# Optimization experiments

Measured on AMD Instinct MI355X. Metric: run time of the kernel, lower is better.

The kernel has to match this reference:

```python
import jax, jax.numpy as jnp
import numpy as np

N, IN_DIM, KEY_DIM, K, VAL_DIM = 100000, 512, 100, 8, 64


def setup_inputs() -> dict:
    key = jax.random.key(0)
    ks = jax.random.split(key, 7)
    s = 0.02
    return {
        "x": jax.random.normal(ks[0], (N, IN_DIM), dtype=jnp.float32),
        "Wk": jax.random.normal(ks[1], (KEY_DIM, IN_DIM), dtype=jnp.float32) * s,
        "bk": jax.random.normal(ks[2], (KEY_DIM,), dtype=jnp.float32) * s,
        "Wq": jax.random.normal(ks[3], (K, KEY_DIM), dtype=jnp.float32) * s,
        "bq": jax.random.normal(ks[4], (K,), dtype=jnp.float32) * s,
        "Wv": jax.random.normal(ks[5], (VAL_DIM, IN_DIM), dtype=jnp.float32) * s,
        "bv": jax.random.normal(ks[6], (VAL_DIM,), dtype=jnp.float32) * s,
    }


def reference(x, Wk, bk, Wq, bq, Wv, bv):
    # torch.nn.Linear: y = x @ W.T + b
    key = x @ Wk.T + bk                  # [N, key_dim]
    val = x @ Wv.T + bv                  # [N, val_dim]
    que = key @ Wq.T + bq                # [N, k]
    # att_norm == 'softmax': per-sample softmax over the k groups
    w = jax.nn.softmax(que, axis=-1)     # [N, k]
    # per-sample outer product w_i^T @ val_i -> [N, k, val_dim]
    x_group = w[:, :, None] * val[:, None, :]
    return x_group
```

## Files before the change

kernel.cpp:

```cpp
#include <hip/hip_runtime.h>

#define NROWS 100000
#define IN_DIM 512

typedef __attribute__((ext_vector_type(8))) short short8;
typedef __attribute__((ext_vector_type(4))) float f32x4;

__device__ inline unsigned short f2bf(float f) {
    union { float f; unsigned u; } v; v.f = f;
    unsigned u = v.u;
    return (unsigned short)((u + 0x7FFFu + ((u >> 16) & 1u)) >> 16);
}

__global__ void qg_prepack(const float* __restrict__ Wk, const float* __restrict__ bk,
                           const float* __restrict__ Wq, const float* __restrict__ bq,
                           const float* __restrict__ Wv,
                           unsigned short* __restrict__ Bp, float* __restrict__ qb) {
    int id = blockIdx.x * 256 + threadIdx.x;
    if (id < 8) {
        float s = bq[id];
        #pragma unroll 4
        for (int j = 0; j < 100; ++j) s += Wq[id * 100 + j] * bk[j];
        qb[id] = s;
    }
    if (id >= 5120) return;
    int lane = id & 63;
    int ks = (id >> 6) & 15;
    int t = id >> 10;
    int c = t * 16 + (lane & 15);
    int kk = ks * 32 + (lane >> 4) * 8;
    short8 pk;
    #pragma unroll
    for (int e = 0; e < 8; ++e) {
        int k2 = kk + e;
        float w;
        if (c < 64) {
            w = Wv[c * IN_DIM + k2];
        } else if (c < 72) {
            float s = 0.f;
            #pragma unroll 4
            for (int j = 0; j < 100; ++j) s += Wq[(c - 64) * 100 + j] * Wk[j * IN_DIM + k2];
            w = s;
        } else {
            w = 0.f;
        }
        pk[e] = (short)f2bf(w);
    }
    ((short8*)Bp)[id] = pk;
}

__global__ __launch_bounds__(128, 4) void qg_main(const float* __restrict__ x,
                                                  const float* __restrict__ bv,
                                                  const unsigned short* __restrict__ Bp,
                                                  const float* __restrict__ qb,
                                                  float* __restrict__ out) {
    __shared__ float vlds[2][16][68];
    __shared__ float wlds[2][16][8];
    const int tid = threadIdx.x;
    const int w = tid >> 6;
    const int lane = tid & 63;
    const int g = lane >> 4;
    const int cl = lane & 15;
    const int rowbase = blockIdx.x * 32 + w * 16;

    const float* ap = x + (size_t)(rowbase + cl) * IN_DIM + g * 8;
    const short8* bp8 = (const short8*)Bp + lane;

    f32x4 acc[5];
    #pragma unroll
    for (int t = 0; t < 5; ++t) acc[t] = (f32x4){0.f, 0.f, 0.f, 0.f};

    float4 A[3][2];
    short8 B[2][5];

    #pragma unroll
    for (int p = 0; p < 3; ++p) {
        A[p][0] = *(const float4*)(ap + p * 32);
        A[p][1] = *(const float4*)(ap + p * 32 + 4);
    }
    #pragma unroll
    for (int p = 0; p < 2; ++p)
        #pragma unroll
        for (int t = 0; t < 5; ++t)
            B[p][t] = bp8[(t * 16 + p) * 64];

    #pragma unroll
    for (int s = 0; s < 16; ++s) {
        const int ai = s % 3, bi = s % 2;
        float4 f0 = A[ai][0];
        float4 f1 = A[ai][1];
        short8 af;
        af[0] = (short)f2bf(f0.x); af[1] = (short)f2bf(f0.y);
        af[2] = (short)f2bf(f0.z); af[3] = (short)f2bf(f0.w);
        af[4] = (short)f2bf(f1.x); af[5] = (short)f2bf(f1.y);
        af[6] = (short)f2bf(f1.z); af[7] = (short)f2bf(f1.w);
        if (s + 3 < 16) {
            A[ai][0] = *(const float4*)(ap + (s + 3) * 32);
            A[ai][1] = *(const float4*)(ap + (s + 3) * 32 + 4);
        }
        #pragma unroll
        for (int t = 0; t < 5; ++t)
            acc[t] = __builtin_amdgcn_mfma_f32_16x16x32_bf16(af, B[bi][t], acc[t], 0, 0, 0);
        if (s + 2 < 16) {
            #pragma unroll
            for (int t = 0; t < 5; ++t)
                B[bi][t] = bp8[(t * 16 + s + 2) * 64];
        }
    }

    #pragma unroll
    for (int t = 0; t < 4; ++t) {
        float b = bv[t * 16 + cl];
        #pragma unroll
        for (int r = 0; r < 4; ++r)
            vlds[w][g * 4 + r][t * 16 + cl] = acc[t][r] + b;
    }
    if (cl < 8) {
        float b = qb[cl];
        #pragma unroll
        for (int r = 0; r < 4; ++r)
            wlds[w][g * 4 + r][cl] = acc[4][r] + b;
    }
    asm volatile("s_waitcnt lgkmcnt(0)" ::: "memory");

    if (lane < 16) {
        float q[8];
        float m = -1e30f;
        #pragma unroll
        for (int k = 0; k < 8; ++k) { q[k] = wlds[w][lane][k]; m = fmaxf(m, q[k]); }
        float ssum = 0.f;
        #pragma unroll
        for (int k = 0; k < 8; ++k) { q[k] = __expf(q[k] - m); ssum += q[k]; }
        float inv = 1.f / ssum;
        #pragma unroll
        for (int k = 0; k < 8; ++k) wlds[w][lane][k] = q[k] * inv;
    }
    asm volatile("s_waitcnt lgkmcnt(0)" ::: "memory");

    f32x4* outp = (f32x4*)out + (size_t)rowbase * 128;
    #pragma unroll
    for (int it = 0; it < 32; ++it) {
        int idx = it * 64 + lane;
        int row = idx >> 7;
        int j = idx & 127;
        float wgt = wlds[w][row][j >> 4];
        float4 vv = *(const float4*)&vlds[w][row][(j & 15) * 4];
        f32x4 o;
        o[0] = wgt * vv.x; o[1] = wgt * vv.y; o[2] = wgt * vv.z; o[3] = wgt * vv.w;
        __builtin_nontemporal_store(o, &outp[(size_t)row * 128 + j]);
    }
}

extern "C" void kernel_launch(void* const* d_in, const int* in_sizes, int n_in,
                              void* d_out, int out_size, void* d_ws, size_t ws_size,
                              hipStream_t stream) {
    const float* x  = (const float*)d_in[0];
    const float* Wk = (const float*)d_in[1];
    const float* bk = (const float*)d_in[2];
    const float* Wq = (const float*)d_in[3];
    const float* bq = (const float*)d_in[4];
    const float* Wv = (const float*)d_in[5];
    const float* bv = (const float*)d_in[6];
    float* out = (float*)d_out;

    unsigned short* Bp = (unsigned short*)d_ws;
    float* qb = (float*)((char*)d_ws + 81920);

    qg_prepack<<<20, 256, 0, stream>>>(Wk, bk, Wq, bq, Wv, Bp, qb);
    qg_main<<<3125, 128, 0, stream>>>(x, bv, Bp, qb, out);
}
```

Measured before the change: 107.1 us.

## Rewrite main GEMM loop in inline asm with 64-row warp tiles

Each wave now processes 64 rows (four 16-row M tiles) instead of 16, so every B fragment load is reused across four MFMA groups. The K loop is hand-written in inline assembly with pinned VGPRs, double-buffered global loads, explicit vmcnt waits and packed bf16 conversion instructions in place of the software rounding. The grid shrinks to 782 blocks and the rows past the end are clamped on load and masked on store. Hard-coded register clobbers and inline asm waits are fragile, and dropping to 2 blocks per CU lowers the occupancy available to hide memory latency in what is a bandwidth-bound kernel.

```diff
diff --git a/kernel.cpp b/kernel.cpp
--- a/kernel.cpp
+++ b/kernel.cpp
@@ -49,105 +49,237 @@
     ((short8*)Bp)[id] = pk;
 }
 
-__global__ __launch_bounds__(128, 4) void qg_main(const float* __restrict__ x,
+#define C32_63  "v32","v33","v34","v35","v36","v37","v38","v39","v40","v41","v42","v43","v44","v45","v46","v47","v48","v49","v50","v51","v52","v53","v54","v55","v56","v57","v58","v59","v60","v61","v62","v63"
+#define C64_95  "v64","v65","v66","v67","v68","v69","v70","v71","v72","v73","v74","v75","v76","v77","v78","v79","v80","v81","v82","v83","v84","v85","v86","v87","v88","v89","v90","v91","v92","v93","v94","v95"
+#define C96_135 "v96","v97","v98","v99","v100","v101","v102","v103","v104","v105","v106","v107","v108","v109","v110","v111","v112","v113","v114","v115","v116","v117","v118","v119","v120","v121","v122","v123","v124","v125","v126","v127","v128","v129","v130","v131","v132","v133","v134","v135"
+#define C136_175 "v136","v137","v138","v139","v140","v141","v142","v143","v144","v145","v146","v147","v148","v149","v150","v151","v152","v153","v154","v155","v156","v157","v158","v159","v160","v161","v162","v163","v164","v165","v166","v167","v168","v169","v170","v171","v172","v173","v174","v175"
+#define C176_215 "v176","v177","v178","v179","v180","v181","v182","v183","v184","v185","v186","v187","v188","v189","v190","v191","v192","v193","v194","v195","v196","v197","v198","v199","v200","v201","v202","v203","v204","v205","v206","v207","v208","v209","v210","v211","v212","v213","v214","v215"
+#define C216_224 "v216","v217","v218","v219","v220","v221","v222","v223","v224"
+#define CLOB C32_63, C64_95, C96_135, C136_175, C176_215, C216_224
+
+#define ISSUE(A0,A1,A2,A3,A4,A5,A6,A7,B0,B1,B2,B3,B4)                          \
+    asm volatile(                                                              \
+        "global_load_dwordx4 " A0 ", v216, %0 offset:0\n\t"                    \
+        "global_load_dwordx4 " A1 ", v216, %0 offset:16\n\t"                   \
+        "v_add_u32 v216, 0x80, v216\n\t"                                       \
+        "global_load_dwordx4 " A2 ", v217, %0 offset:0\n\t"                    \
+        "global_load_dwordx4 " A3 ", v217, %0 offset:16\n\t"                   \
+        "v_add_u32 v217, 0x80, v217\n\t"                                       \
+        "global_load_dwordx4 " A4 ", v218, %0 offset:0\n\t"                    \
+        "global_load_dwordx4 " A5 ", v218, %0 offset:16\n\t"                   \
+        "v_add_u32 v218, 0x80, v218\n\t"                                       \
+        "global_load_dwordx4 " A6 ", v219, %0 offset:0\n\t"                    \
+        "global_load_dwordx4 " A7 ", v219, %0 offset:16\n\t"                   \
+        "v_add_u32 v219, 0x80, v219\n\t"                                       \
+        "global_load_dwordx4 " B0 ", v220, %1 offset:0\n\t"                    \
+        "v_add_u32 v220, 0x400, v220\n\t"                                      \
+        "global_load_dwordx4 " B1 ", v221, %1 offset:0\n\t"                    \
+        "v_add_u32 v221, 0x400, v221\n\t"                                      \
+        "global_load_dwordx4 " B2 ", v222, %1 offset:0\n\t"                    \
+        "v_add_u32 v222, 0x400, v222\n\t"                                      \
+        "global_load_dwordx4 " B3 ", v223, %1 offset:0\n\t"                    \
+        "v_add_u32 v223, 0x400, v223\n\t"                                      \
+        "global_load_dwordx4 " B4 ", v224, %1 offset:0\n\t"                    \
+        "v_add_u32 v224, 0x400, v224"                                          \
+        :: "s"(x), "s"(Bp) : "memory", CLOB)
+
+#define ISSUE0 ISSUE("v[32:35]","v[36:39]","v[40:43]","v[44:47]","v[48:51]","v[52:55]","v[56:59]","v[60:63]", \
+                     "v[96:99]","v[100:103]","v[104:107]","v[108:111]","v[112:115]")
+#define ISSUE1 ISSUE("v[64:67]","v[68:71]","v[72:75]","v[76:79]","v[80:83]","v[84:87]","v[88:91]","v[92:95]", \
+                     "v[116:119]","v[120:123]","v[124:127]","v[128:131]","v[132:135]")
+
+#define MFMA5(AF, B0,B1,B2,B3,B4, ACC0,ACC1,ACC2,ACC3,ACC4)                    \
+        "v_mfma_f32_16x16x32_bf16 " ACC0 ", " AF ", " B0 ", " ACC0 "\n\t"      \
+        "v_mfma_f32_16x16x32_bf16 " ACC1 ", " AF ", " B1 ", " ACC1 "\n\t"      \
+        "v_mfma_f32_16x16x32_bf16 " ACC2 ", " AF ", " B2 ", " ACC2 "\n\t"      \
+        "v_mfma_f32_16x16x32_bf16 " ACC3 ", " AF ", " B3 ", " ACC3 "\n\t"      \
+        "v_mfma_f32_16x16x32_bf16 " ACC4 ", " AF ", " B4 ", " ACC4 "\n\t"
+
+#define CVT4(d0,s0,s1, d1,s2,s3, d2,s4,s5, d3,s6,s7)                           \
+        "v_cvt_pk_bf16_f32 " d0 ", " s0 ", " s1 "\n\t"                         \
+        "v_cvt_pk_bf16_f32 " d1 ", " s2 ", " s3 "\n\t"                         \
+        "v_cvt_pk_bf16_f32 " d2 ", " s4 ", " s5 "\n\t"                         \
+        "v_cvt_pk_bf16_f32 " d3 ", " s6 ", " s7 "\n\t"
+
+#define CONS0(NW)                                                              \
+    asm volatile("s_waitcnt vmcnt(" NW ")" ::: "memory");                      \
+    asm volatile(                                                              \
+        CVT4("v32","v32","v33","v33","v34","v35","v34","v36","v37","v35","v38","v39") \
+        CVT4("v40","v40","v41","v41","v42","v43","v42","v44","v45","v43","v46","v47") \
+        CVT4("v48","v48","v49","v49","v50","v51","v50","v52","v53","v51","v54","v55") \
+        CVT4("v56","v56","v57","v57","v58","v59","v58","v60","v61","v59","v62","v63") \
+        "s_nop 1\n\t"                                                          \
+        MFMA5("v[32:35]","v[96:99]","v[100:103]","v[104:107]","v[108:111]","v[112:115]", \
+              "v[136:139]","v[140:143]","v[144:147]","v[148:151]","v[152:155]") \
+        MFMA5("v[40:43]","v[96:99]","v[100:103]","v[104:107]","v[108:111]","v[112:115]", \
+              "v[156:159]","v[160:163]","v[164:167]","v[168:171]","v[172:175]") \
+        MFMA5("v[48:51]","v[96:99]","v[100:103]","v[104:107]","v[108:111]","v[112:115]", \
+              "v[176:179]","v[180:183]","v[184:187]","v[188:191]","v[192:195]") \
+        MFMA5("v[56:59]","v[96:99]","v[100:103]","v[104:107]","v[108:111]","v[112:115]", \
+              "v[196:199]","v[200:203]","v[204:207]","v[208:211]","v[212:215]") \
+        "s_nop 0" ::: "memory", CLOB)
+
+#define CONS1(NW)                                                              \
+    asm volatile("s_waitcnt vmcnt(" NW ")" ::: "memory");                      \
+    asm volatile(                                                              \
+        CVT4("v64","v64","v65","v65","v66","v67","v66","v68","v69","v67","v70","v71") \
+        CVT4("v72","v72","v73","v73","v74","v75","v74","v76","v77","v75","v78","v79") \
+        CVT4("v80","v80","v81","v81","v82","v83","v82","v84","v85","v83","v86","v87") \
+        CVT4("v88","v88","v89","v89","v90","v91","v90","v92","v93","v91","v94","v95") \
+        "s_nop 1\n\t"                                                          \
+        MFMA5("v[64:67]","v[116:119]","v[120:123]","v[124:127]","v[128:131]","v[132:135]", \
+              "v[136:139]","v[140:143]","v[144:147]","v[148:151]","v[152:155]") \
+        MFMA5("v[72:75]","v[116:119]","v[120:123]","v[124:127]","v[128:131]","v[132:135]", \
+              "v[156:159]","v[160:163]","v[164:167]","v[168:171]","v[172:175]") \
+        MFMA5("v[80:83]","v[116:119]","v[120:123]","v[124:127]","v[128:131]","v[132:135]", \
+              "v[176:179]","v[180:183]","v[184:187]","v[188:191]","v[192:195]") \
+        MFMA5("v[88:91]","v[116:119]","v[120:123]","v[124:127]","v[128:131]","v[132:135]", \
+              "v[196:199]","v[200:203]","v[204:207]","v[208:211]","v[212:215]") \
+        "s_nop 0" ::: "memory", CLOB)
+
+__global__ __launch_bounds__(128, 2) void qg_main(const float* __restrict__ x,
                                                   const float* __restrict__ bv,
                                                   const unsigned short* __restrict__ Bp,
                                                   const float* __restrict__ qb,
                                                   float* __restrict__ out) {
-    __shared__ float vlds[2][16][68];
-    __shared__ float wlds[2][16][8];
+    __shared__ float epi[2][64][76];
     const int tid = threadIdx.x;
     const int w = tid >> 6;
     const int lane = tid & 63;
     const int g = lane >> 4;
     const int cl = lane & 15;
-    const int rowbase = blockIdx.x * 32 + w * 16;
-
-    const float* ap = x + (size_t)(rowbase + cl) * IN_DIM + g * 8;
-    const short8* bp8 = (const short8*)Bp + lane;
-
-    f32x4 acc[5];
-    #pragma unroll
-    for (int t = 0; t < 5; ++t) acc[t] = (f32x4){0.f, 0.f, 0.f, 0.f};
-
-    float4 A[3][2];
-    short8 B[2][5];
-
-    #pragma unroll
-    for (int p = 0; p < 3; ++p) {
-        A[p][0] = *(const float4*)(ap + p * 32);
-        A[p][1] = *(const float4*)(ap + p * 32 + 4);
-    }
-    #pragma unroll
-    for (int p = 0; p < 2; ++p)
+    const int rowbase = blockIdx.x * 128 + w * 64;
+
+    unsigned voffA[4];
+    #pragma unroll
+    for (int m = 0; m < 4; ++m)
+        voffA[m] = (unsigned)(min(rowbase + m * 16 + cl, NROWS - 1) * 512 + g * 8) * 4u;
+    const unsigned voffB = (unsigned)lane * 16u;
+
+    float bvr[4];
+    #pragma unroll
+    for (int t = 0; t < 4; ++t) bvr[t] = bv[t * 16 + cl];
+    float qbr = qb[cl & 7];
+    asm volatile("s_waitcnt vmcnt(0)" ::: "memory");
+
+    asm volatile(
+        "v_mov_b32 v216, %0\n\tv_mov_b32 v217, %1\n\t"
+        "v_mov_b32 v218, %2\n\tv_mov_b32 v219, %3\n\t"
+        "v_mov_b32 v220, %4\n\tv_mov_b32 v221, %5\n\t"
+        "v_mov_b32 v222, %6\n\tv_mov_b32 v223, %7\n\t"
+        "v_mov_b32 v224, %8"
+        :: "v"(voffA[0]), "v"(voffA[1]), "v"(voffA[2]), "v"(voffA[3]),
+           "v"(voffB), "v"(voffB + 16384u), "v"(voffB + 32768u),
+           "v"(voffB + 49152u), "v"(voffB + 65536u)
+        : CLOB);
+    {
+        char zbuf[1];  (void)zbuf;
+        asm volatile(
+            "v_mov_b32 v136, 0\n\tv_mov_b32 v137, 0\n\tv_mov_b32 v138, 0\n\tv_mov_b32 v139, 0\n\t"
+            "v_mov_b32 v140, 0\n\tv_mov_b32 v141, 0\n\tv_mov_b32 v142, 0\n\tv_mov_b32 v143, 0\n\t"
+            "v_mov_b32 v144, 0\n\tv_mov_b32 v145, 0\n\tv_mov_b32 v146, 0\n\tv_mov_b32 v147, 0\n\t"
+            "v_mov_b32 v148, 0\n\tv_mov_b32 v149, 0\n\tv_mov_b32 v150, 0\n\tv_mov_b32 v151, 0\n\t"
+            "v_mov_b32 v152, 0\n\tv_mov_b32 v153, 0\n\tv_mov_b32 v154, 0\n\tv_mov_b32 v155, 0\n\t"
+            "v_mov_b32 v156, 0\n\tv_mov_b32 v157, 0\n\tv_mov_b32 v158, 0\n\tv_mov_b32 v159, 0\n\t"
+            "v_mov_b32 v160, 0\n\tv_mov_b32 v161, 0\n\tv_mov_b32 v162, 0\n\tv_mov_b32 v163, 0\n\t"
+            "v_mov_b32 v164, 0\n\tv_mov_b32 v165, 0\n\tv_mov_b32 v166, 0\n\tv_mov_b32 v167, 0\n\t"
+            "v_mov_b32 v168, 0\n\tv_mov_b32 v169, 0\n\tv_mov_b32 v170, 0\n\tv_mov_b32 v171, 0\n\t"
+            "v_mov_b32 v172, 0\n\tv_mov_b32 v173, 0\n\tv_mov_b32 v174, 0\n\tv_mov_b32 v175, 0\n\t"
+            "v_mov_b32 v176, 0\n\tv_mov_b32 v177, 0\n\tv_mov_b32 v178, 0\n\tv_mov_b32 v179, 0\n\t"
+            "v_mov_b32 v180, 0\n\tv_mov_b32 v181, 0\n\tv_mov_b32 v182, 0\n\tv_mov_b32 v183, 0\n\t"
+            "v_mov_b32 v184, 0\n\tv_mov_b32 v185, 0\n\tv_mov_b32 v186, 0\n\tv_mov_b32 v187, 0\n\t"
+            "v_mov_b32 v188, 0\n\tv_mov_b32 v189, 0\n\tv_mov_b32 v190, 0\n\tv_mov_b32 v191, 0\n\t"
+            "v_mov_b32 v192, 0\n\tv_mov_b32 v193, 0\n\tv_mov_b32 v194, 0\n\tv_mov_b32 v195, 0\n\t"
+            "v_mov_b32 v196, 0\n\tv_mov_b32 v197, 0\n\tv_mov_b32 v198, 0\n\tv_mov_b32 v199, 0\n\t"
+            "v_mov_b32 v200, 0\n\tv_mov_b32 v201, 0\n\tv_mov_b32 v202, 0\n\tv_mov_b32 v203, 0\n\t"
+            "v_mov_b32 v204, 0\n\tv_mov_b32 v205, 0\n\tv_mov_b32 v206, 0\n\tv_mov_b32 v207, 0\n\t"
+            "v_mov_b32 v208, 0\n\tv_mov_b32 v209, 0\n\tv_mov_b32 v210, 0\n\tv_mov_b32 v211, 0\n\t"
+            "v_mov_b32 v212, 0\n\tv_mov_b32 v213, 0\n\tv_mov_b32 v214, 0\n\tv_mov_b32 v215, 0"
+            ::: CLOB);
+    }
+
+    ISSUE0; ISSUE1;
+    CONS0("13"); ISSUE0;
+    CONS1("13"); ISSUE1;
+    CONS0("13"); ISSUE0;
+    CONS1("13"); ISSUE1;
+    CONS0("13"); ISSUE0;
+    CONS1("13"); ISSUE1;
+    CONS0("13"); ISSUE0;
+    CONS1("13"); ISSUE1;
+    CONS0("13"); ISSUE0;
+    CONS1("13"); ISSUE1;
+    CONS0("13"); ISSUE0;
+    CONS1("13"); ISSUE1;
+    CONS0("13"); ISSUE0;
+    CONS1("13"); ISSUE1;
+    CONS0("13");
+    CONS1("0");
+
+    asm volatile("s_nop 7\n\ts_nop 7\n\ts_nop 7");
+    float ac[4][5][4];
+    #define EXT(M, T, R0, R1, R2, R3)                                          \
+        asm volatile("v_mov_b32 %0, " R0 "\n\tv_mov_b32 %1, " R1 "\n\t"        \
+                     "v_mov_b32 %2, " R2 "\n\tv_mov_b32 %3, " R3               \
+                     : "=v"(ac[M][T][0]), "=v"(ac[M][T][1]),                   \
+                       "=v"(ac[M][T][2]), "=v"(ac[M][T][3]))
+    EXT(0,0,"v136","v137","v138","v139"); EXT(0,1,"v140","v141","v142","v143");
+    EXT(0,2,"v144","v145","v146","v147"); EXT(0,3,"v148","v149","v150","v151");
+    EXT(0,4,"v152","v153","v154","v155");
+    EXT(1,0,"v156","v157","v158","v159"); EXT(1,1,"v160","v161","v162","v163");
+    EXT(1,2,"v164","v165","v166","v167"); EXT(1,3,"v168","v169","v170","v171");
+    EXT(1,4,"v172","v173","v174","v175");
+    EXT(2,0,"v176","v177","v178","v179"); EXT(2,1,"v180","v181","v182","v183");
+    EXT(2,2,"v184","v185","v186","v187"); EXT(2,3,"v188","v189","v190","v191");
+    EXT(2,4,"v192","v193","v194","v195");
+    EXT(3,0,"v196","v197","v198","v199"); EXT(3,1,"v200","v201","v202","v203");
+    EXT(3,2,"v204","v205","v206","v207"); EXT(3,4,"v212","v213","v214","v215");
+    EXT(3,3,"v208","v209","v210","v211");
+    #undef EXT
+
+    #pragma unroll
+    for (int m = 0; m < 4; ++m) {
         #pragma unroll
-        for (int t = 0; t < 5; ++t)
-            B[p][t] = bp8[(t * 16 + p) * 64];
-
-    #pragma unroll
-    for (int s = 0; s < 16; ++s) {
-        const int ai = s % 3, bi = s % 2;
-        float4 f0 = A[ai][0];
-        float4 f1 = A[ai][1];
-        short8 af;
-        af[0] = (short)f2bf(f0.x); af[1] = (short)f2bf(f0.y);
-        af[2] = (short)f2bf(f0.z); af[3] = (short)f2bf(f0.w);
-        af[4] = (short)f2bf(f1.x); af[5] = (short)f2bf(f1.y);
-        af[6] = (short)f2bf(f1.z); af[7] = (short)f2bf(f1.w);
-        if (s + 3 < 16) {
-            A[ai][0] = *(const float4*)(ap + (s + 3) * 32);
-            A[ai][1] = *(const float4*)(ap + (s + 3) * 32 + 4);
+        for (int t = 0; t < 4; ++t) {
+            #pragma unroll
+            for (int r = 0; r < 4; ++r)
+                epi[w][m * 16 + g * 4 + r][t * 16 + cl] = ac[m][t][r] + bvr[t];
         }
-        #pragma unroll
-        for (int t = 0; t < 5; ++t)
-            acc[t] = __builtin_amdgcn_mfma_f32_16x16x32_bf16(af, B[bi][t], acc[t], 0, 0, 0);
-        if (s + 2 < 16) {
+        if (cl < 8) {
             #pragma unroll
-            for (int t = 0; t < 5; ++t)
-                B[bi][t] = bp8[(t * 16 + s + 2) * 64];
+            for (int r = 0; r < 4; ++r)
+                epi[w][m * 16 + g * 4 + r][64 + cl] = ac[m][4][r] + qbr;
         }
     }
-
-    #pragma unroll
-    for (int t = 0; t < 4; ++t) {
-        float b = bv[t * 16 + cl];
-        #pragma unroll
-        for (int r = 0; r < 4; ++r)
-            vlds[w][g * 4 + r][t * 16 + cl] = acc[t][r] + b;
-    }
-    if (cl < 8) {
-        float b = qb[cl];
-        #pragma unroll
-        for (int r = 0; r < 4; ++r)
-            wlds[w][g * 4 + r][cl] = acc[4][r] + b;
-    }
     asm volatile("s_waitcnt lgkmcnt(0)" ::: "memory");
 
-    if (lane < 16) {
+    {
         float q[8];
         float m = -1e30f;
         #pragma unroll
-        for (int k = 0; k < 8; ++k) { q[k] = wlds[w][lane][k]; m = fmaxf(m, q[k]); }
+        for (int k = 0; k < 8; ++k) { q[k] = epi[w][lane][64 + k]; m = fmaxf(m, q[k]); }
         float ssum = 0.f;
         #pragma unroll
         for (int k = 0; k < 8; ++k) { q[k] = __expf(q[k] - m); ssum += q[k]; }
         float inv = 1.f / ssum;
         #pragma unroll
-        for (int k = 0; k < 8; ++k) wlds[w][lane][k] = q[k] * inv;
+        for (int k = 0; k < 8; ++k) epi[w][lane][64 + k] = q[k] * inv;
     }
     asm volatile("s_waitcnt lgkmcnt(0)" ::: "memory");
 
     f32x4* outp = (f32x4*)out + (size_t)rowbase * 128;
     #pragma unroll
-    for (int it = 0; it < 32; ++it) {
+    for (int it = 0; it < 128; ++it) {
         int idx = it * 64 + lane;
         int row = idx >> 7;
         int j = idx & 127;
-        float wgt = wlds[w][row][j >> 4];
-        float4 vv = *(const float4*)&vlds[w][row][(j & 15) * 4];
-        f32x4 o;
-        o[0] = wgt * vv.x; o[1] = wgt * vv.y; o[2] = wgt * vv.z; o[3] = wgt * vv.w;
-        __builtin_nontemporal_store(o, &outp[(size_t)row * 128 + j]);
+        if (rowbase + row < NROWS) {
+            float wgt = epi[w][row][64 + (j >> 4)];
+            float4 vv = *(const float4*)&epi[w][row][(j & 15) * 4];
+            f32x4 o;
+            o[0] = wgt * vv.x; o[1] = wgt * vv.y; o[2] = wgt * vv.z; o[3] = wgt * vv.w;
+            __builtin_nontemporal_store(o, &outp[(size_t)row * 128 + j]);
+        }
     }
 }
 
@@ -167,5 +299,5 @@
     float* qb = (float*)((char*)d_ws + 81920);
 
     qg_prepack<<<20, 256, 0, stream>>>(Wk, bk, Wq, bq, Wv, Bp, qb);
-    qg_main<<<3125, 128, 0, stream>>>(x, bv, Bp, qb, out);
+    qg_main<<<782, 128, 0, stream>>>(x, bv, Bp, qb, out);
 }
```

Measured after the change: 102.3 us. 1.05x faster.
